# Kernel optimization log

Hardware: AMD Instinct MI355X
Metric: run time of the kernel (lower is better)

Reference implementation:

```python
import jax, jax.numpy as jnp
import numpy as np
from jax import lax

DN = ('NCHW', 'OIHW', 'NCHW')

def _score(x, dw_w, dw_b, pw_w, pw_b):
    C = x.shape[1]
    # depthwise 3x3 conv (groups=C), padding=1
    h = lax.conv_general_dilated(x, dw_w, (1, 1), 'SAME', dimension_numbers=DN,
                                 feature_group_count=C)
    h = h + dw_b[None, :, None, None]
    # 1x1 conv C->1
    s = lax.conv_general_dilated(h, pw_w, (1, 1), 'SAME', dimension_numbers=DN)
    s = s + pw_b[None, :, None, None]
    return jax.nn.sigmoid(s)  # [B,1,H,W]


def setup_inputs() -> dict:
    key = jax.random.key(0)
    ks = jax.random.split(key, 8)
    B, C, H, W = 8, 64, 256, 256
    inp = {
        'x0': jax.random.normal(ks[0], (B, C, H, W), jnp.float32),
        'x1': jax.random.normal(ks[1], (B, C, H, W), jnp.float32),
        'dw_w0': jax.random.normal(ks[2], (C, 1, 3, 3), jnp.float32) * 0.1,
        'dw_b0': jnp.zeros((C,), jnp.float32),
        'pw_w0': jax.random.normal(ks[3], (1, C, 1, 1), jnp.float32) * 0.1,
        'pw_b0': jnp.zeros((1,), jnp.float32),
        'dw_w1': jax.random.normal(ks[4], (C, 1, 3, 3), jnp.float32) * 0.1,
        'dw_b1': jnp.zeros((C,), jnp.float32),
        'pw_w1': jax.random.normal(ks[5], (1, C, 1, 1), jnp.float32) * 0.1,
        'pw_b1': jnp.zeros((1,), jnp.float32),
    }
    return inp


def reference(x0, x1, dw_w0, dw_b0, pw_w0, pw_b0, dw_w1, dw_b1, pw_w1, pw_b1):
    s0 = _score(x0, dw_w0, dw_b0, pw_w0, pw_b0)  # [B,1,H,W]
    s1 = _score(x1, dw_w1, dw_b1, pw_w1, pw_b1)
    w0 = s0 * x0 + x0  # [B,C,H,W]
    w1 = s1 * x1 + x1
    stacked = jnp.stack([w0, w1])            # [2,B,C,H,W]
    idx = jnp.argmax(stacked, axis=0)        # [B,C,H,W] int
    x_f = jnp.where(idx == 0, x0, x1)
    percentages = jnp.stack([jnp.mean((idx == i).astype(jnp.float32)) for i in range(2)])
    return x_f, percentages
```

## Files before the change

kernel.cpp:

```cpp
#include <hip/hip_runtime.h>
#include <math.h>
#include <stdint.h>

#define B 8
#define C 64
#define H 256
#define W 256
#define NPLANE 16
#define PSZ (H * W)

#define OFF_WC    256
#define OFF_BIAS  9728
#define OFF_PART  16384

__global__ void prep_kernel(const float* __restrict__ dw_w0, const float* __restrict__ dw_b0,
                            const float* __restrict__ pw_w0, const float* __restrict__ pw_b0,
                            const float* __restrict__ dw_w1, const float* __restrict__ dw_b1,
                            const float* __restrict__ pw_w1, const float* __restrict__ pw_b1,
                            double* __restrict__ wc, double* __restrict__ bias)
{
    int t = threadIdx.x;
    int which = t >> 6, c = t & 63;
    const float* dw = which ? dw_w1 : dw_w0;
    const float* pw = which ? pw_w1 : pw_w0;
    double p = (double)pw[c];
    #pragma unroll
    for (int k = 0; k < 9; ++k)
        wc[(which * 64 + c) * 9 + k] = p * (double)dw[c * 9 + k];
    if (c == 0) {
        const float* dwb = which ? dw_b1 : dw_b0;
        const float* pwb = which ? pw_b1 : pw_b0;
        double acc = (double)pwb[0];
        for (int cc = 0; cc < 64; ++cc) acc += (double)pw[cc] * (double)dwb[cc];
        bias[which] = acc;
    }
}

template<int JLO, int JHI>
__device__ __forceinline__ void accum_q(
    const float* __restrict__ xb,
    const double* __restrict__ w9,
    const int gy[4], int lane, double acc[2][4])
{
    #pragma unroll 1
    for (int cc = 0; cc < 16; ++cc) {
        const float* xc = xb + (size_t)cc * PSZ;
        float4 r0 = *(const float4*)(xc + gy[0]);
        float4 r1 = *(const float4*)(xc + gy[1]);
        float4 r2 = *(const float4*)(xc + gy[2]);
        float4 r3 = *(const float4*)(xc + gy[3]);

        double wl[9];
        #pragma unroll
        for (int t = 0; t < 9; ++t) wl[t] = w9[cc * 9 + t];

        const float4 rr[4] = {r0, r1, r2, r3};
        #pragma unroll
        for (int j = 0; j < 4; ++j) {
            if (j < JLO || j > JHI) continue;
            float lf = __shfl_up(rr[j].w, 1);
            float rf = __shfl_down(rr[j].x, 1);
            if (lane == 0)  lf = 0.0f;
            if (lane == 63) rf = 0.0f;
            double dd[6] = {(double)lf, (double)rr[j].x, (double)rr[j].y,
                            (double)rr[j].z, (double)rr[j].w, (double)rf};
            #pragma unroll
            for (int i = 0; i < 3; ++i) {
                const int o = j - i;
                if (o >= 0 && o < 2) {
                    double wa = wl[3 * i], wb = wl[3 * i + 1], wcv = wl[3 * i + 2];
                    #pragma unroll
                    for (int k = 0; k < 4; ++k)
                        acc[o][k] += wa * dd[k] + wb * dd[k + 1] + wcv * dd[k + 2];
                }
            }
        }
    }
}

__global__ __launch_bounds__(64) void score_part_kernel(
    const float* __restrict__ x0, const float* __restrict__ x1,
    const double* __restrict__ wc, double* __restrict__ part)
{
    const int n    = blockIdx.x;
    const int task = (n & 7) * 1024 + (n >> 3);
    const int plane = task >> 9;
    const int band  = (task >> 2) & 127;
    const int q     = task & 3;
    const int which = plane >> 3;
    const int b     = plane & 7;
    const int y0    = band * 2;

    const int lane = threadIdx.x;

    const float*  xb = (which ? x1 : x0) + (size_t)b * C * PSZ
                     + (size_t)(q * 16) * PSZ + lane * 4;
    const double* w9 = wc + which * (C * 9) + (q * 16) * 9;

    int gy[4];
    #pragma unroll
    for (int j = 0; j < 4; ++j) {
        int r = y0 - 1 + j;
        r = r < 0 ? 0 : (r > H - 1 ? H - 1 : r);
        gy[j] = r * W;
    }

    double acc[2][4] = {};

    if (band == 0)        accum_q<1, 3>(xb, w9, gy, lane, acc);
    else if (band == 127) accum_q<0, 2>(xb, w9, gy, lane, acc);
    else                  accum_q<0, 3>(xb, w9, gy, lane, acc);

    double* pp = part + ((size_t)plane * 4 + q) * PSZ + (size_t)y0 * W + lane * 4;
    #pragma unroll
    for (int o = 0; o < 2; ++o) {
        double2* row = (double2*)(pp + o * W);
        row[0] = make_double2(acc[o][0], acc[o][1]);
        row[1] = make_double2(acc[o][2], acc[o][3]);
    }
}

__global__ __launch_bounds__(256) void select_kernel(
    const float*  __restrict__ x0,
    const float*  __restrict__ x1,
    const double* __restrict__ part,
    const double* __restrict__ bias,
    float* __restrict__ out,
    unsigned int* __restrict__ count1)
{
    const int by = blockIdx.x;
    const int b  = by >> 8;
    const int y  = by & (H - 1);
    const int tx = threadIdx.x & 63;
    const int tc = threadIdx.x >> 6;

    const size_t rowoff = (size_t)y * W + (size_t)tx * 4;
    double s0[4] = {}, s1[4] = {};
    #pragma unroll
    for (int q = 0; q < 4; ++q) {
        const double* p0 = part + ((size_t)b * 4 + q) * PSZ + rowoff;
        const double* p1 = part + ((size_t)(8 + b) * 4 + q) * PSZ + rowoff;
        #pragma unroll
        for (int j = 0; j < 4; ++j) { s0[j] += p0[j]; s1[j] += p1[j]; }
    }
    const double bv0 = bias[0], bv1 = bias[1];
    double g0[4], g1[4];
    #pragma unroll
    for (int j = 0; j < 4; ++j) {
        g0[j] = 1.0 + 1.0 / (1.0 + exp(-(s0[j] + bv0)));
        g1[j] = 1.0 + 1.0 / (1.0 + exp(-(s1[j] + bv1)));
    }

    const size_t rowbase = (size_t)b * C * H * W + rowoff;

    unsigned int cnt = 0;
    for (int ci = tc; ci < C; ci += 4) {
        size_t off = rowbase + (size_t)ci * H * W;
        float4 a  = *(const float4*)(x0 + off);
        float4 bb = *(const float4*)(x1 + off);
        float4 r;
        { double w0=(double)a.x*g0[0], w1=(double)bb.x*g1[0]; bool s1_=(w1>w0); cnt+=s1_; r.x=s1_?bb.x:a.x; }
        { double w0=(double)a.y*g0[1], w1=(double)bb.y*g1[1]; bool s1_=(w1>w0); cnt+=s1_; r.y=s1_?bb.y:a.y; }
        { double w0=(double)a.z*g0[2], w1=(double)bb.z*g1[2]; bool s1_=(w1>w0); cnt+=s1_; r.z=s1_?bb.z:a.z; }
        { double w0=(double)a.w*g0[3], w1=(double)bb.w*g1[3]; bool s1_=(w1>w0); cnt+=s1_; r.w=s1_?bb.w:a.w; }
        *(float4*)(out + off) = r;
    }

    __shared__ unsigned int blk;
    if (threadIdx.x == 0) blk = 0;
    __syncthreads();
    atomicAdd(&blk, cnt);
    __syncthreads();
    if (threadIdx.x == 0) atomicAdd(count1, blk);
}

__global__ void finalize_kernel(const unsigned int* __restrict__ count1,
                                float* __restrict__ out_p)
{
    const double N = (double)B * C * H * W;
    double c1 = (double)(*count1);
    out_p[0] = (float)((N - c1) / N);
    out_p[1] = (float)(c1 / N);
}

extern "C" void kernel_launch(void* const* d_in, const int* in_sizes, int n_in,
                              void* d_out, int out_size, void* d_ws, size_t ws_size,
                              hipStream_t stream) {
    const float* x0    = (const float*)d_in[0];
    const float* x1    = (const float*)d_in[1];
    const float* dw_w0 = (const float*)d_in[2];
    const float* dw_b0 = (const float*)d_in[3];
    const float* pw_w0 = (const float*)d_in[4];
    const float* pw_b0 = (const float*)d_in[5];
    const float* dw_w1 = (const float*)d_in[6];
    const float* dw_b1 = (const float*)d_in[7];
    const float* pw_w1 = (const float*)d_in[8];
    const float* pw_b1 = (const float*)d_in[9];
    float* out = (float*)d_out;

    unsigned int* cnt  = (unsigned int*)d_ws;
    double*       wc   = (double*)((char*)d_ws + OFF_WC);
    double*       bias = (double*)((char*)d_ws + OFF_BIAS);
    double*       part = (double*)((char*)d_ws + OFF_PART);

    (void)hipMemsetAsync(d_ws, 0, 256, stream);

    prep_kernel<<<1, 128, 0, stream>>>(dw_w0, dw_b0, pw_w0, pw_b0,
                                       dw_w1, dw_b1, pw_w1, pw_b1, wc, bias);

    score_part_kernel<<<NPLANE * 128 * 4, 64, 0, stream>>>(x0, x1, wc, part);

    select_kernel<<<B * H, 256, 0, stream>>>(x0, x1, part, bias, out, cnt);

    finalize_kernel<<<1, 1, 0, stream>>>(cnt, out + (size_t)B * C * H * W);
}
```

Before: 159.5 us.

## Fuse score computation and selection into one kernel with shared-memory reduction

Merges the partial-score kernel and the select kernel into a single 512-thread block per (batch, 2-row band). Eight waves compute channel-chunk partial scores for both inputs, reduce them through shared memory, apply the sigmoid, then reuse the gates to select outputs for those two rows across all channels. This drops the large double-precision partial-score buffer and its global write and read-back, and the separate launch. In exchange there are fewer blocks (1024), heavier per-block register and LDS use, and block-level syncs between the compute and select phases.

```diff
diff --git a/kernel.cpp b/kernel.cpp
--- a/kernel.cpp
+++ b/kernel.cpp
@@ -6,12 +6,10 @@
 #define C 64
 #define H 256
 #define W 256
-#define NPLANE 16
 #define PSZ (H * W)
 
 #define OFF_WC    256
 #define OFF_BIAS  9728
-#define OFF_PART  16384
 
 __global__ void prep_kernel(const float* __restrict__ dw_w0, const float* __restrict__ dw_b0,
                             const float* __restrict__ pw_w0, const float* __restrict__ pw_b0,
@@ -78,24 +76,31 @@
     }
 }
 
-__global__ __launch_bounds__(64) void score_part_kernel(
+__global__ __launch_bounds__(512) void fused_kernel(
     const float* __restrict__ x0, const float* __restrict__ x1,
-    const double* __restrict__ wc, double* __restrict__ part)
-{
+    const double* __restrict__ wc, const double* __restrict__ bias,
+    float* __restrict__ out, unsigned int* __restrict__ count1)
+{
+    __shared__ double sred[2][4][2][4][64];
+    __shared__ unsigned int scnt;
+
     const int n    = blockIdx.x;
-    const int task = (n & 7) * 1024 + (n >> 3);
-    const int plane = task >> 9;
-    const int band  = (task >> 2) & 127;
-    const int q     = task & 3;
-    const int which = plane >> 3;
-    const int b     = plane & 7;
-    const int y0    = band * 2;
-
-    const int lane = threadIdx.x;
-
-    const float*  xb = (which ? x1 : x0) + (size_t)b * C * PSZ
-                     + (size_t)(q * 16) * PSZ + lane * 4;
-    const double* w9 = wc + which * (C * 9) + (q * 16) * 9;
+    const int task = (n & 7) * 128 + (n >> 3);
+    const int b    = task >> 7;
+    const int band = task & 127;
+    const int y0   = band * 2;
+
+    const int tid   = threadIdx.x;
+    const int w     = tid >> 6;
+    const int lane  = tid & 63;
+    const int which = w >> 2;
+    const int chunk = w & 3;
+
+    if (tid == 0) scnt = 0;
+
+    const float* xin = which ? x1 : x0;
+    const float* xb  = xin + (size_t)b * C * PSZ + (size_t)(chunk * 16) * PSZ + lane * 4;
+    const double* w9 = wc + which * (C * 9) + (chunk * 16) * 9;
 
     int gy[4];
     #pragma unroll
@@ -111,67 +116,70 @@
     else if (band == 127) accum_q<0, 2>(xb, w9, gy, lane, acc);
     else                  accum_q<0, 3>(xb, w9, gy, lane, acc);
 
-    double* pp = part + ((size_t)plane * 4 + q) * PSZ + (size_t)y0 * W + lane * 4;
-    #pragma unroll
-    for (int o = 0; o < 2; ++o) {
-        double2* row = (double2*)(pp + o * W);
-        row[0] = make_double2(acc[o][0], acc[o][1]);
-        row[1] = make_double2(acc[o][2], acc[o][3]);
-    }
-}
-
-__global__ __launch_bounds__(256) void select_kernel(
-    const float*  __restrict__ x0,
-    const float*  __restrict__ x1,
-    const double* __restrict__ part,
-    const double* __restrict__ bias,
-    float* __restrict__ out,
-    unsigned int* __restrict__ count1)
-{
-    const int by = blockIdx.x;
-    const int b  = by >> 8;
-    const int y  = by & (H - 1);
-    const int tx = threadIdx.x & 63;
-    const int tc = threadIdx.x >> 6;
-
-    const size_t rowoff = (size_t)y * W + (size_t)tx * 4;
-    double s0[4] = {}, s1[4] = {};
-    #pragma unroll
-    for (int q = 0; q < 4; ++q) {
-        const double* p0 = part + ((size_t)b * 4 + q) * PSZ + rowoff;
-        const double* p1 = part + ((size_t)(8 + b) * 4 + q) * PSZ + rowoff;
-        #pragma unroll
-        for (int j = 0; j < 4; ++j) { s0[j] += p0[j]; s1[j] += p1[j]; }
-    }
-    const double bv0 = bias[0], bv1 = bias[1];
-    double g0[4], g1[4];
-    #pragma unroll
-    for (int j = 0; j < 4; ++j) {
-        g0[j] = 1.0 + 1.0 / (1.0 + exp(-(s0[j] + bv0)));
-        g1[j] = 1.0 + 1.0 / (1.0 + exp(-(s1[j] + bv1)));
-    }
-
-    const size_t rowbase = (size_t)b * C * H * W + rowoff;
+    #pragma unroll
+    for (int o = 0; o < 2; ++o)
+        #pragma unroll
+        for (int k = 0; k < 4; ++k)
+            sred[which][chunk][o][k][lane] = acc[o][k];
+    __syncthreads();
+
+    double fv0, fv1;
+    {
+        int idx = tid;
+        int wh = idx >> 9, row = (idx >> 8) & 1, px = idx & 255;
+        int k = px & 3, l = px >> 2;
+        double s = sred[wh][0][row][k][l] + sred[wh][1][row][k][l]
+                 + sred[wh][2][row][k][l] + sred[wh][3][row][k][l] + bias[wh];
+        fv0 = 1.0 + 1.0 / (1.0 + exp(-s));
+    }
+    {
+        int idx = 512 + tid;
+        int wh = idx >> 9, row = (idx >> 8) & 1, px = idx & 255;
+        int k = px & 3, l = px >> 2;
+        double s = sred[wh][0][row][k][l] + sred[wh][1][row][k][l]
+                 + sred[wh][2][row][k][l] + sred[wh][3][row][k][l] + bias[wh];
+        fv1 = 1.0 + 1.0 / (1.0 + exp(-s));
+    }
+    __syncthreads();
+
+    double* sf = &sred[0][0][0][0][0];
+    sf[tid] = fv0;
+    sf[512 + tid] = fv1;
+    __syncthreads();
+
+    const int tx = tid & 63;
+    const int tc = tid >> 6;
+
+    double g0[2][4], g1[2][4];
+    #pragma unroll
+    for (int row = 0; row < 2; ++row)
+        #pragma unroll
+        for (int j = 0; j < 4; ++j) {
+            g0[row][j] = sf[row * 256 + tx * 4 + j];
+            g1[row][j] = sf[512 + row * 256 + tx * 4 + j];
+        }
 
     unsigned int cnt = 0;
-    for (int ci = tc; ci < C; ci += 4) {
-        size_t off = rowbase + (size_t)ci * H * W;
-        float4 a  = *(const float4*)(x0 + off);
-        float4 bb = *(const float4*)(x1 + off);
-        float4 r;
-        { double w0=(double)a.x*g0[0], w1=(double)bb.x*g1[0]; bool s1_=(w1>w0); cnt+=s1_; r.x=s1_?bb.x:a.x; }
-        { double w0=(double)a.y*g0[1], w1=(double)bb.y*g1[1]; bool s1_=(w1>w0); cnt+=s1_; r.y=s1_?bb.y:a.y; }
-        { double w0=(double)a.z*g0[2], w1=(double)bb.z*g1[2]; bool s1_=(w1>w0); cnt+=s1_; r.z=s1_?bb.z:a.z; }
-        { double w0=(double)a.w*g0[3], w1=(double)bb.w*g1[3]; bool s1_=(w1>w0); cnt+=s1_; r.w=s1_?bb.w:a.w; }
-        *(float4*)(out + off) = r;
-    }
-
-    __shared__ unsigned int blk;
-    if (threadIdx.x == 0) blk = 0;
-    __syncthreads();
-    atomicAdd(&blk, cnt);
-    __syncthreads();
-    if (threadIdx.x == 0) atomicAdd(count1, blk);
+    const size_t base = (size_t)b * C * PSZ + (size_t)y0 * W + (size_t)tx * 4;
+    #pragma unroll 1
+    for (int ci = tc; ci < C; ci += 8) {
+        #pragma unroll
+        for (int row = 0; row < 2; ++row) {
+            size_t off = base + (size_t)ci * PSZ + (size_t)row * W;
+            float4 a  = *(const float4*)(x0 + off);
+            float4 bb = *(const float4*)(x1 + off);
+            float4 r;
+            { double v0=(double)a.x*g0[row][0], v1=(double)bb.x*g1[row][0]; bool s1=(v1>v0); cnt+=s1; r.x=s1?bb.x:a.x; }
+            { double v0=(double)a.y*g0[row][1], v1=(double)bb.y*g1[row][1]; bool s1=(v1>v0); cnt+=s1; r.y=s1?bb.y:a.y; }
+            { double v0=(double)a.z*g0[row][2], v1=(double)bb.z*g1[row][2]; bool s1=(v1>v0); cnt+=s1; r.z=s1?bb.z:a.z; }
+            { double v0=(double)a.w*g0[row][3], v1=(double)bb.w*g1[row][3]; bool s1=(v1>v0); cnt+=s1; r.w=s1?bb.w:a.w; }
+            *(float4*)(out + off) = r;
+        }
+    }
+
+    atomicAdd(&scnt, cnt);
+    __syncthreads();
+    if (tid == 0) atomicAdd(count1, scnt);
 }
 
 __global__ void finalize_kernel(const unsigned int* __restrict__ count1,
@@ -201,16 +209,13 @@
     unsigned int* cnt  = (unsigned int*)d_ws;
     double*       wc   = (double*)((char*)d_ws + OFF_WC);
     double*       bias = (double*)((char*)d_ws + OFF_BIAS);
-    double*       part = (double*)((char*)d_ws + OFF_PART);
 
     (void)hipMemsetAsync(d_ws, 0, 256, stream);
 
     prep_kernel<<<1, 128, 0, stream>>>(dw_w0, dw_b0, pw_w0, pw_b0,
                                        dw_w1, dw_b1, pw_w1, pw_b1, wc, bias);
 
-    score_part_kernel<<<NPLANE * 128 * 4, 64, 0, stream>>>(x0, x1, wc, part);
-
-    select_kernel<<<B * H, 256, 0, stream>>>(x0, x1, part, bias, out, cnt);
+    fused_kernel<<<B * (H / 2), 512, 0, stream>>>(x0, x1, wc, bias, out, cnt);
 
     finalize_kernel<<<1, 1, 0, stream>>>(cnt, out + (size_t)B * C * H * W);
 }
```

Measured after the change: 133.0 us. -16.6%, faster.
